# Performance work log

Hardware: AMD Instinct MI355X
Metric: run time of the kernel (lower is better)

Reference implementation:

```python
import jax, jax.numpy as jnp
import numpy as np

N_EXPERTS = 8
TOP_K = 2
AUX_COEF = 0.01
Z_COEF = 0.001


def setup_inputs() -> dict:
    key = jax.random.key(0)
    ks = jax.random.split(key, 5)
    B, S, D, F, E = 2, 2048, 768, 2048, N_EXPERTS
    std = 0.02
    std_out = std / np.sqrt(2 * 12)  # scale_init_by_depth, n_layers=12
    return {
        "x": jax.random.normal(ks[0], (B, S, D), jnp.float32),
        "router_w": jax.random.normal(ks[1], (D, E), jnp.float32) * std,
        "w1": jax.random.normal(ks[2], (E, D, F), jnp.float32) * std,
        "w2": jax.random.normal(ks[3], (E, F, D), jnp.float32) * std_out,
        "w3": jax.random.normal(ks[4], (E, D, F), jnp.float32) * std,
    }


def reference(x, router_w, w1, w2, w3):
    B, S, D = x.shape
    E = w1.shape[0]
    x_flat = x.reshape(-1, D)                      # [N, D]
    n_tokens = x_flat.shape[0]

    router_logits = x_flat @ router_w               # [N, E]
    probs = jax.nn.softmax(router_logits.astype(jnp.float32), axis=-1)
    topk_w, topk_i = jax.lax.top_k(probs, TOP_K)    # [N, K]
    topk_w = topk_w / jnp.sum(topk_w, axis=-1, keepdims=True)

    # Combine: equivalent to sort/group dispatch + per-expert GEMM + index_add,
    # expressed as a masked per-expert (fixed, small E) dense pass.
    out = jnp.zeros((n_tokens, D), dtype=x.dtype)
    for e in range(E):
        gate = jnp.sum(jnp.where(topk_i == e, topk_w, 0.0), axis=-1)  # [N] f32
        h = jax.nn.silu(x_flat @ w1[e]) * (x_flat @ w3[e])            # [N, F]
        out = out + gate[:, None].astype(x.dtype) * (h @ w2[e])

    # Switch-style load-balancing aux loss + z-loss
    importance = probs.mean(axis=0)                 # [E]
    top1 = topk_i[:, 0]
    load = jnp.zeros((E,), jnp.float32).at[top1].add(1.0) / n_tokens
    aux_loss = E * jnp.sum(importance * load) * AUX_COEF
    z_loss = jnp.mean(router_logits.astype(jnp.float32) ** 2) * Z_COEF

    return out.reshape(B, S, D), aux_loss, z_loss
```

## Files before the change

### kernel.cpp

```cpp
#include <hip/hip_runtime.h>
#include <hip/hip_bf16.h>

constexpr int NT = 4096;
constexpr int DD = 768;
constexpr int FF = 2048;
constexpr int NE = 8;
constexpr int MAXROWS = 9216;
constexpr int MAXMT128 = 72;

constexpr int IDX_CNTA   = 0;
constexpr int IDX_CNTT1  = 8;
constexpr int IDX_CUR    = 16;
constexpr int IDX_IMP    = 24;
constexpr int IDX_ZSUM   = 32;
constexpr int IDX_NTILES = 33;
constexpr int IDX_OFF    = 34;
constexpr int IDX_EXPT   = 48;

constexpr size_t OFF_META   = 0;
constexpr size_t OFF_TKE    = 1024;
constexpr size_t OFF_GATE   = OFF_TKE    + (size_t)NT*2*4;
constexpr size_t OFF_ROWOF  = OFF_GATE   + (size_t)NT*2*4;
constexpr size_t OFF_TOKROW = OFF_ROWOF  + (size_t)NT*2*4;
constexpr size_t OFF_XG     = 136192;
constexpr size_t OFF_W1T    = OFF_XG  + (size_t)MAXROWS*DD*2;
constexpr size_t OFF_W3T    = OFF_W1T + (size_t)NE*FF*DD*2;
constexpr size_t OFF_W2T    = OFF_W3T + (size_t)NE*FF*DD*2;
constexpr size_t OFF_H      = OFF_W2T + (size_t)NE*FF*DD*2;
constexpr size_t OFF_OP     = OFF_H   + (size_t)MAXROWS*FF*2;

typedef float f32x4 __attribute__((ext_vector_type(4)));
typedef __bf16 bf16x8v __attribute__((ext_vector_type(8)));
typedef unsigned short u16x8 __attribute__((ext_vector_type(8)));

__device__ inline unsigned short f2bf_bits(float f) {
  __bf16 h = (__bf16)f;
  return *(unsigned short*)&h;
}
__device__ inline float bf2f(unsigned short u) {
  unsigned v = (unsigned)u << 16;
  return *(float*)&v;
}

__device__ __forceinline__ void glds16(const void* g, void* l) {
  __builtin_amdgcn_global_load_lds(
      (const __attribute__((address_space(1))) unsigned int*)g,
      (__attribute__((address_space(3))) unsigned int*)l, 16, 0, 0);
}

constexpr int RB = 128;
__global__ __launch_bounds__(256) void router_kernel(const float* __restrict__ x,
    const float* __restrict__ rw, int* __restrict__ meta,
    int* __restrict__ tke, float* __restrict__ gateArr,
    int* __restrict__ tokrow) {
  const int gtid = blockIdx.x * 256 + threadIdx.x;
  if (gtid < MAXROWS) tokrow[gtid] = -1;

  __shared__ float s_imp[NE];
  __shared__ float s_z;
  __shared__ int s_cnt1[NE], s_cnta[NE];
  if (threadIdx.x < NE) { s_imp[threadIdx.x] = 0.f; s_cnt1[threadIdx.x] = 0; s_cnta[threadIdx.x] = 0; }
  if (threadIdx.x == 0) s_z = 0.f;
  __syncthreads();

  const int wave = threadIdx.x >> 6, lane = threadIdx.x & 63;
  float impacc[NE];
  #pragma unroll
  for (int e = 0; e < NE; ++e) impacc[e] = 0.f;
  float zacc = 0.f;

  for (int t = blockIdx.x * 4 + wave; t < NT; t += RB * 4) {
    float acc[NE];
    #pragma unroll
    for (int e = 0; e < NE; ++e) acc[e] = 0.f;
    const float* xr = x + (size_t)t * DD;
    for (int i = lane; i < DD / 4; i += 64) {
      float4 xv = ((const float4*)xr)[i];
      const float* r = rw + i * 4 * NE;
      #pragma unroll
      for (int e = 0; e < NE; ++e) acc[e] += xv.x * r[e];
      #pragma unroll
      for (int e = 0; e < NE; ++e) acc[e] += xv.y * r[NE + e];
      #pragma unroll
      for (int e = 0; e < NE; ++e) acc[e] += xv.z * r[2*NE + e];
      #pragma unroll
      for (int e = 0; e < NE; ++e) acc[e] += xv.w * r[3*NE + e];
    }
    #pragma unroll
    for (int off = 32; off > 0; off >>= 1) {
      #pragma unroll
      for (int e = 0; e < NE; ++e) acc[e] += __shfl_xor(acc[e], off);
    }
    float mx = acc[0];
    #pragma unroll
    for (int e = 1; e < NE; ++e) mx = fmaxf(mx, acc[e]);
    float p[NE]; float s = 0.f;
    #pragma unroll
    for (int e = 0; e < NE; ++e) { p[e] = __expf(acc[e] - mx); s += p[e]; }
    float inv = 1.f / s;
    #pragma unroll
    for (int e = 0; e < NE; ++e) p[e] *= inv;
    int e0 = 0; float p0 = p[0];
    #pragma unroll
    for (int e = 1; e < NE; ++e) if (p[e] > p0) { p0 = p[e]; e0 = e; }
    int e1 = -1; float p1 = -1.f;
    #pragma unroll
    for (int e = 0; e < NE; ++e) if (e != e0 && p[e] > p1) { p1 = p[e]; e1 = e; }
    if (lane == 0) {
      #pragma unroll
      for (int e = 0; e < NE; ++e) { impacc[e] += p[e]; zacc += acc[e] * acc[e]; }
      atomicAdd(&s_cnt1[e0], 1);
      atomicAdd(&s_cnta[e0], 1);
      atomicAdd(&s_cnta[e1], 1);
      float gs = 1.f / (p0 + p1);
      tke[t*2]   = e0; tke[t*2+1] = e1;
      gateArr[t*2] = p0 * gs; gateArr[t*2+1] = p1 * gs;
    }
  }
  if (lane == 0) {
    #pragma unroll
    for (int e = 0; e < NE; ++e) atomicAdd(&s_imp[e], impacc[e]);
    atomicAdd(&s_z, zacc);
  }
  __syncthreads();
  float* fmeta = (float*)meta;
  if (threadIdx.x < NE) {
    atomicAdd(&fmeta[IDX_IMP + threadIdx.x], s_imp[threadIdx.x]);
    atomicAdd(&meta[IDX_CNTT1 + threadIdx.x], s_cnt1[threadIdx.x]);
    atomicAdd(&meta[IDX_CNTA + threadIdx.x], s_cnta[threadIdx.x]);
  }
  if (threadIdx.x == NE) atomicAdd(&fmeta[IDX_ZSUM], s_z);
}

__global__ __launch_bounds__(128) void scan_kernel(int* __restrict__ meta,
                                                   float* __restrict__ out_tail) {
  __shared__ int s_off[NE + 1];
  __shared__ int s_nt[NE];
  __shared__ float s_aux;
  const int t = threadIdx.x;
  if (t < NE) s_nt[t] = (meta[IDX_CNTA + t] + 127) >> 7;
  __syncthreads();
  if (t == 0) {
    int off = 0;
    for (int e = 0; e < NE; ++e) { s_off[e] = off; off += s_nt[e]; }
    s_off[NE] = off;
  }
  __syncthreads();
  const int ntiles = s_off[NE];
  if (t < NE) meta[IDX_OFF + t] = s_off[t] << 7;
  if (t == NE) { meta[IDX_OFF + NE] = ntiles << 7; meta[IDX_NTILES] = ntiles; }
  if (t < ntiles) {
    int e = 0;
    while (t >= s_off[e + 1]) e++;
    meta[IDX_EXPT + t] = e;
  }
  float* fmeta = (float*)meta;
  float pl = 0.f;
  if (t < NE)
    pl = (fmeta[IDX_IMP + t] / (float)NT) * ((float)meta[IDX_CNTT1 + t] / (float)NT);
  if (t < 64) {
    #pragma unroll
    for (int off = 4; off > 0; off >>= 1) pl += __shfl_xor(pl, off);
    if (t == 0) s_aux = pl;
  }
  __syncthreads();
  if (t == 0) {
    out_tail[0] = (float)NE * s_aux * 0.01f;
    out_tail[1] = fmeta[IDX_ZSUM] / (float)(NT * NE) * 0.001f;
  }
}

__global__ __launch_bounds__(256) void scatter_kernel(const int* __restrict__ tke,
    int* __restrict__ meta, int* __restrict__ rowof, int* __restrict__ tokrow) {
  __shared__ int s_cnt[NE], s_base[NE];
  const int t = blockIdx.x * 256 + threadIdx.x;
  if (threadIdx.x < NE) s_cnt[threadIdx.x] = 0;
  __syncthreads();
  const int e0 = tke[t*2], e1 = tke[t*2 + 1];
  const int l0 = atomicAdd(&s_cnt[e0], 1);
  const int l1 = atomicAdd(&s_cnt[e1], 1);
  __syncthreads();
  if (threadIdx.x < NE)
    s_base[threadIdx.x] = atomicAdd(&meta[IDX_CUR + threadIdx.x], s_cnt[threadIdx.x]);
  __syncthreads();
  const int r0 = meta[IDX_OFF + e0] + s_base[e0] + l0;
  const int r1 = meta[IDX_OFF + e1] + s_base[e1] + l1;
  rowof[t*2]     = r0;
  rowof[t*2 + 1] = r1;
  tokrow[r0] = t;
  tokrow[r1] = t;
}

__global__ __launch_bounds__(192) void gather_kernel(const float* __restrict__ x,
    const int* __restrict__ tokrow, const int* __restrict__ meta,
    __bf16* __restrict__ Xg) {
  const int row = blockIdx.x;
  if (row >= meta[IDX_OFF + NE]) return;
  const int tok = tokrow[row];
  ushort4* dst = (ushort4*)(Xg + (size_t)row * DD);
  const int i = threadIdx.x;
  ushort4 o;
  if (tok >= 0) {
    float4 v = ((const float4*)(x + (size_t)tok * DD))[i];
    o.x = f2bf_bits(v.x); o.y = f2bf_bits(v.y);
    o.z = f2bf_bits(v.z); o.w = f2bf_bits(v.w);
  } else {
    o.x = o.y = o.z = o.w = 0;
  }
  dst[i] = o;
}

constexpr int TS = 68;
__global__ __launch_bounds__(256) void transpose_cvt_all(
    const float* __restrict__ w1, const float* __restrict__ w3,
    const float* __restrict__ w2, __bf16* __restrict__ W1t,
    __bf16* __restrict__ W3t, __bf16* __restrict__ W2t,
    int* __restrict__ meta) {
  if (blockIdx.x == 0 && blockIdx.y == 0 && blockIdx.z == 0)
    meta[threadIdx.x] = 0;

  const int z = blockIdx.z, which = z >> 3, e = z & 7;
  const float* src; __bf16* dst; int R, C;
  int r0a, c0a, r0b, c0b;
  if (which == 0)      { src = w1; dst = W1t; R = DD; C = FF;
                         r0a = blockIdx.y * 64; c0a = blockIdx.x * 128;
                         r0b = r0a;             c0b = c0a + 64; }
  else if (which == 1) { src = w3; dst = W3t; R = DD; C = FF;
                         r0a = blockIdx.y * 64; c0a = blockIdx.x * 128;
                         r0b = r0a;             c0b = c0a + 64; }
  else                 { src = w2; dst = W2t; R = FF; C = DD;
                         r0a = blockIdx.x * 128; c0a = blockIdx.y * 64;
                         r0b = r0a + 64;         c0b = c0a; }
  src += (size_t)e * DD * FF; dst += (size_t)e * DD * FF;
  __shared__ __align__(16) __bf16 tile[64 * TS];
  const int t = threadIdx.x;
  const int rr = t >> 4, qq = t & 15;

  float4 va[4], vb[4];
  #pragma unroll
  for (int i = 0; i < 4; ++i)
    va[i] = *(const float4*)&src[(size_t)(r0a + rr + i * 16) * C + c0a + qq * 4];
  #pragma unroll
  for (int i = 0; i < 4; ++i)
    vb[i] = *(const float4*)&src[(size_t)(r0b + rr + i * 16) * C + c0b + qq * 4];

  #pragma unroll
  for (int i = 0; i < 4; ++i) {
    ushort4 o;
    o.x = f2bf_bits(va[i].x); o.y = f2bf_bits(va[i].y);
    o.z = f2bf_bits(va[i].z); o.w = f2bf_bits(va[i].w);
    *(ushort4*)&tile[(rr + i * 16) * TS + qq * 4] = o;
  }
  __syncthreads();
  #pragma unroll
  for (int i = 0; i < 2; ++i) {
    int idx = t + i * 256; int c = idx >> 3, seg = idx & 7;
    u16x8 o;
    #pragma unroll
    for (int k = 0; k < 8; ++k)
      o[k] = *(unsigned short*)&tile[(seg * 8 + k) * TS + c];
    *(u16x8*)&dst[(size_t)(c0a + c) * R + r0a + seg * 8] = o;
  }
  __syncthreads();

  #pragma unroll
  for (int i = 0; i < 4; ++i) {
    ushort4 o;
    o.x = f2bf_bits(vb[i].x); o.y = f2bf_bits(vb[i].y);
    o.z = f2bf_bits(vb[i].z); o.w = f2bf_bits(vb[i].w);
    *(ushort4*)&tile[(rr + i * 16) * TS + qq * 4] = o;
  }
  __syncthreads();
  #pragma unroll
  for (int i = 0; i < 2; ++i) {
    int idx = t + i * 256; int c = idx >> 3, seg = idx & 7;
    u16x8 o;
    #pragma unroll
    for (int k = 0; k < 8; ++k)
      o[k] = *(unsigned short*)&tile[(seg * 8 + k) * TS + c];
    *(u16x8*)&dst[(size_t)(c0b + c) * R + r0b + seg * 8] = o;
  }
}

__global__ __launch_bounds__(256) void gemm1_kernel(const __bf16* __restrict__ Xg,
    const __bf16* __restrict__ W1t, const __bf16* __restrict__ W3t,
    __bf16* __restrict__ Hb, const int* __restrict__ meta) {
  const int mt = blockIdx.y;
  if (mt >= meta[IDX_NTILES]) return;
  const int e = meta[IDX_EXPT + mt];
  const int n0 = blockIdx.x * 64;
  const int m0 = mt * 128;
  __shared__ __align__(16) __bf16 As[128*32], B1s[64*32], B3s[64*32];
  const int t = threadIdx.x, wave = t >> 6, lane = t & 63;
  const __bf16* w1e = W1t + (size_t)e * FF * DD;
  const __bf16* w3e = W3t + (size_t)e * FF * DD;
  const f32x4 zero = {0.f, 0.f, 0.f, 0.f};
  f32x4 acc1[2][4], acc3[2][4];
  #pragma unroll
  for (int i = 0; i < 2; ++i)
    #pragma unroll
    for (int j = 0; j < 4; ++j) { acc1[i][j] = zero; acc3[i][j] = zero; }

  const __bf16* gA  = Xg  + (size_t)(m0 + 32*wave + (lane >> 2)) * DD + (lane & 3) * 8;
  const __bf16* gB1 = w1e + (size_t)(n0 + 16*wave + (lane >> 2)) * DD + (lane & 3) * 8;
  const __bf16* gB3 = w3e + (size_t)(n0 + 16*wave + (lane >> 2)) * DD + (lane & 3) * 8;
  __bf16* lA0 = &As [(32*wave     ) * 32];
  __bf16* lA1 = &As [(32*wave + 16) * 32];
  __bf16* lB1 = &B1s[(16*wave     ) * 32];
  __bf16* lB3 = &B3s[(16*wave     ) * 32];

  for (int k0 = 0; k0 < DD; k0 += 32) {
    glds16(gA  + k0,           lA0);
    glds16(gA  + k0 + 16*DD,   lA1);
    glds16(gB1 + k0,           lB1);
    glds16(gB3 + k0,           lB3);
    __syncthreads();
    bf16x8v a[2], b1[4], b3[4];
    #pragma unroll
    for (int i = 0; i < 2; ++i)
      a[i] = *(const bf16x8v*)&As[(32*wave + 16*i + (lane & 15))*32 + (lane >> 4)*8];
    #pragma unroll
    for (int j = 0; j < 4; ++j) {
      b1[j] = *(const bf16x8v*)&B1s[(16*j + (lane & 15))*32 + (lane >> 4)*8];
      b3[j] = *(const bf16x8v*)&B3s[(16*j + (lane & 15))*32 + (lane >> 4)*8];
    }
    #pragma unroll
    for (int i = 0; i < 2; ++i)
      #pragma unroll
      for (int j = 0; j < 4; ++j) {
        acc1[i][j] = __builtin_amdgcn_mfma_f32_16x16x32_bf16(a[i], b1[j], acc1[i][j], 0, 0, 0);
        acc3[i][j] = __builtin_amdgcn_mfma_f32_16x16x32_bf16(a[i], b3[j], acc3[i][j], 0, 0, 0);
      }
    __syncthreads();
  }
  #pragma unroll
  for (int i = 0; i < 2; ++i) {
    const int rowb = m0 + 32*wave + 16*i + (lane >> 4)*4;
    #pragma unroll
    for (int j = 0; j < 4; ++j) {
      const int col = n0 + 16*j + (lane & 15);
      #pragma unroll
      for (int r = 0; r < 4; ++r) {
        float c1 = acc1[i][j][r], c3 = acc3[i][j][r];
        float h = c1 / (1.f + __expf(-c1)) * c3;
        Hb[(size_t)(rowb + r)*FF + col] = (__bf16)h;
      }
    }
  }
}

__global__ __launch_bounds__(256) void gemm2_kernel(const __bf16* __restrict__ Hb,
    const __bf16* __restrict__ W2t, __bf16* __restrict__ OP,
    const int* __restrict__ meta) {
  const int mt = blockIdx.y;
  if (mt >= meta[IDX_NTILES]) return;
  const int e = meta[IDX_EXPT + mt];
  const int n0 = blockIdx.x * 128;
  const int m0 = mt * 128;
  __shared__ __align__(16) __bf16 As[128*32], Bs[128*32];
  const int t = threadIdx.x, wave = t >> 6, lane = t & 63;
  const int wm = wave & 1, wn = wave >> 1;
  const __bf16* w2e = W2t + (size_t)e * DD * FF;
  const f32x4 zero = {0.f, 0.f, 0.f, 0.f};
  f32x4 acc[4][4];
  #pragma unroll
  for (int i = 0; i < 4; ++i)
    #pragma unroll
    for (int j = 0; j < 4; ++j) acc[i][j] = zero;

  const __bf16* gA = Hb  + (size_t)(m0 + 32*wave + (lane >> 2)) * FF + (lane & 3) * 8;
  const __bf16* gB = w2e + (size_t)(n0 + 32*wave + (lane >> 2)) * FF + (lane & 3) * 8;
  __bf16* lA0 = &As[(32*wave     ) * 32];
  __bf16* lA1 = &As[(32*wave + 16) * 32];
  __bf16* lB0 = &Bs[(32*wave     ) * 32];
  __bf16* lB1 = &Bs[(32*wave + 16) * 32];

  for (int k0 = 0; k0 < FF; k0 += 32) {
    glds16(gA + k0,          lA0);
    glds16(gA + k0 + 16*FF,  lA1);
    glds16(gB + k0,          lB0);
    glds16(gB + k0 + 16*FF,  lB1);
    __syncthreads();
    bf16x8v a[4], b[4];
    #pragma unroll
    for (int i = 0; i < 4; ++i) {
      a[i] = *(const bf16x8v*)&As[(64*wm + 16*i + (lane & 15))*32 + (lane >> 4)*8];
      b[i] = *(const bf16x8v*)&Bs[(64*wn + 16*i + (lane & 15))*32 + (lane >> 4)*8];
    }
    #pragma unroll
    for (int i = 0; i < 4; ++i)
      #pragma unroll
      for (int j = 0; j < 4; ++j)
        acc[i][j] = __builtin_amdgcn_mfma_f32_16x16x32_bf16(a[i], b[j], acc[i][j], 0, 0, 0);
    __syncthreads();
  }
  #pragma unroll
  for (int i = 0; i < 4; ++i) {
    const int rowb = m0 + 64*wm + 16*i + (lane >> 4)*4;
    #pragma unroll
    for (int j = 0; j < 4; ++j) {
      const int col = n0 + 64*wn + 16*j + (lane & 15);
      #pragma unroll
      for (int r = 0; r < 4; ++r)
        OP[(size_t)(rowb + r)*DD + col] = (__bf16)acc[i][j][r];
    }
  }
}

__global__ __launch_bounds__(192) void combine_kernel(const __bf16* __restrict__ OP,
    const int* __restrict__ rowof, const float* __restrict__ gateArr,
    float* __restrict__ out) {
  const int t = blockIdx.x;
  const int r0 = rowof[t*2], r1 = rowof[t*2 + 1];
  const float g0 = gateArr[t*2], g1 = gateArr[t*2 + 1];
  const ushort4* p0 = (const ushort4*)(OP + (size_t)r0 * DD);
  const ushort4* p1 = (const ushort4*)(OP + (size_t)r1 * DD);
  const int i = threadIdx.x;
  ushort4 a = p0[i], b = p1[i];
  float4 o;
  o.x = g0 * bf2f(a.x) + g1 * bf2f(b.x);
  o.y = g0 * bf2f(a.y) + g1 * bf2f(b.y);
  o.z = g0 * bf2f(a.z) + g1 * bf2f(b.z);
  o.w = g0 * bf2f(a.w) + g1 * bf2f(b.w);
  ((float4*)(out + (size_t)t * DD))[i] = o;
}

extern "C" void kernel_launch(void* const* d_in, const int* in_sizes, int n_in,
                              void* d_out, int out_size, void* d_ws, size_t ws_size,
                              hipStream_t stream) {
  const float* x  = (const float*)d_in[0];
  const float* rw = (const float*)d_in[1];
  const float* w1 = (const float*)d_in[2];
  const float* w2 = (const float*)d_in[3];
  const float* w3 = (const float*)d_in[4];
  float* out = (float*)d_out;

  char* ws = (char*)d_ws;
  int*    meta   = (int*)(ws + OFF_META);
  int*    tke    = (int*)(ws + OFF_TKE);
  float*  gateA  = (float*)(ws + OFF_GATE);
  int*    rowof  = (int*)(ws + OFF_ROWOF);
  int*    tokrow = (int*)(ws + OFF_TOKROW);
  __bf16* Xg     = (__bf16*)(ws + OFF_XG);
  __bf16* W1t    = (__bf16*)(ws + OFF_W1T);
  __bf16* W3t    = (__bf16*)(ws + OFF_W3T);
  __bf16* W2t    = (__bf16*)(ws + OFF_W2T);
  __bf16* Hb     = (__bf16*)(ws + OFF_H);
  __bf16* OP     = (__bf16*)(ws + OFF_OP);

  transpose_cvt_all<<<dim3(16, 12, 24), 256, 0, stream>>>(w1, w3, w2,
                                                          W1t, W3t, W2t, meta);
  router_kernel<<<RB, 256, 0, stream>>>(x, rw, meta, tke, gateA, tokrow);
  scan_kernel<<<1, 128, 0, stream>>>(meta, out + (size_t)NT * DD);
  scatter_kernel<<<NT/256, 256, 0, stream>>>(tke, meta, rowof, tokrow);
  gather_kernel<<<MAXROWS, 192, 0, stream>>>(x, tokrow, meta, Xg);

  gemm1_kernel<<<dim3(FF/64, MAXMT128), 256, 0, stream>>>(Xg, W1t, W3t, Hb, meta);
  gemm2_kernel<<<dim3(DD/128, MAXMT128), 256, 0, stream>>>(Hb, W2t, OP, meta);
  combine_kernel<<<NT, 192, 0, stream>>>(OP, rowof, gateA, out);
}
```

Measured before the change: 352.9 us.

## Rewrite gemm2 with 256x128 tiles, double-buffered LDS and swizzled layout

The down-projection GEMM now uses 512-thread blocks computing 256x128 tiles with BK=64. The scan kernel builds a per-expert 256-row tile table, and a row limit masks stores that would spill into the next expert. Global-to-LDS loads are double-buffered with explicit vmcnt waits, LDS is XOR-swizzled to avoid bank conflicts, and s_setprio is raised around the MFMA bursts. The goal is more reuse of each W2 load, fewer barriers per FLOP and overlap of loads with compute, at the cost of more padded work in partially filled tiles and higher register and LDS use.

```diff
diff --git a/kernel.cpp b/kernel.cpp
--- a/kernel.cpp
+++ b/kernel.cpp
@@ -7,6 +7,8 @@
 constexpr int NE = 8;
 constexpr int MAXROWS = 9216;
 constexpr int MAXMT128 = 72;
+constexpr int MAXMT256 = 40;
+constexpr int NKT2 = FF / 64;
 
 constexpr int IDX_CNTA   = 0;
 constexpr int IDX_CNTT1  = 8;
@@ -16,6 +18,10 @@
 constexpr int IDX_NTILES = 33;
 constexpr int IDX_OFF    = 34;
 constexpr int IDX_EXPT   = 48;
+constexpr int IDX_N256   = 120;
+constexpr int IDX_E256   = 128;
+constexpr int IDX_B256   = 168;
+constexpr int IDX_L256   = 208;
 
 constexpr size_t OFF_META   = 0;
 constexpr size_t OFF_TKE    = 1024;
@@ -153,6 +159,21 @@
     int e = 0;
     while (t >= s_off[e + 1]) e++;
     meta[IDX_EXPT + t] = e;
+  }
+  if (t == 0) {
+    int n2t = 0;
+    for (int e = 0; e < NE; ++e) {
+      const int base = s_off[e] << 7;
+      const int lim  = base + (s_nt[e] << 7);
+      const int n2 = (s_nt[e] + 1) >> 1;
+      for (int i = 0; i < n2; ++i) {
+        meta[IDX_E256 + n2t] = e;
+        meta[IDX_B256 + n2t] = base + (i << 8);
+        meta[IDX_L256 + n2t] = lim;
+        ++n2t;
+      }
+    }
+    meta[IDX_N256] = n2t;
   }
   float* fmeta = (float*)meta;
   float pl = 0.f;
@@ -349,60 +370,136 @@
   }
 }
 
-__global__ __launch_bounds__(256) void gemm2_kernel(const __bf16* __restrict__ Hb,
-    const __bf16* __restrict__ W2t, __bf16* __restrict__ OP,
-    const int* __restrict__ meta) {
+__global__ __launch_bounds__(512, 2) void gemm2_kernel(
+    const __bf16* __restrict__ Hb, const __bf16* __restrict__ W2t,
+    __bf16* __restrict__ OP, const int* __restrict__ meta) {
   const int mt = blockIdx.y;
-  if (mt >= meta[IDX_NTILES]) return;
-  const int e = meta[IDX_EXPT + mt];
+  if (mt >= meta[IDX_N256]) return;
+  const int e      = meta[IDX_E256 + mt];
+  const int m0     = meta[IDX_B256 + mt];
+  const int rowlim = meta[IDX_L256 + mt];
   const int n0 = blockIdx.x * 128;
-  const int m0 = mt * 128;
-  __shared__ __align__(16) __bf16 As[128*32], Bs[128*32];
-  const int t = threadIdx.x, wave = t >> 6, lane = t & 63;
-  const int wm = wave & 1, wn = wave >> 1;
-  const __bf16* w2e = W2t + (size_t)e * DD * FF;
+
+  __shared__ __align__(16) __bf16 As[2][256 * 64];
+  __shared__ __align__(16) __bf16 Bs[2][128 * 64];
+
+  const int t = threadIdx.x, lane = t & 63, wid = t >> 6;
+  const int wm = wid >> 2, wn = wid & 3;
+  const int lane15 = lane & 15, g = lane >> 4;
+
+  const __bf16* __restrict__ W2e = W2t + (size_t)e * DD * FF;
+
+  const int aBase = (wm * 128 + lane15) * 64;
+  const int bBase = (wn * 32 + lane15) * 64;
+  const int c0 = ((g    ) ^ (lane & 7)) * 8;
+  const int c1 = ((4 + g) ^ (lane & 7)) * 8;
+
+  const int o0v = t, o1v = 512 + t;
+  const int r0v = o0v >> 3, r1v = o1v >> 3;
+  const int cl0 = (o0v & 7) ^ (r0v & 7), cl1 = (o1v & 7) ^ (r1v & 7);
+  const int L00 = (       wid * 64) * 8;
+  const int L01 = ( 512 + wid * 64) * 8;
+  const int L10 = (1024 + wid * 64) * 8;
+  const int L11 = (1536 + wid * 64) * 8;
+
+  int gA00 = m0 + r0v;        if (gA00 >= MAXROWS) gA00 = 0;
+  int gA01 = m0 + r1v;        if (gA01 >= MAXROWS) gA01 = 0;
+  int gA10 = m0 + 128 + r0v;  if (gA10 >= MAXROWS) gA10 = 0;
+  int gA11 = m0 + 128 + r1v;  if (gA11 >= MAXROWS) gA11 = 0;
+  const __bf16* aS00 = Hb + (size_t)gA00 * FF + cl0 * 8;
+  const __bf16* aS01 = Hb + (size_t)gA01 * FF + cl1 * 8;
+  const __bf16* aS10 = Hb + (size_t)gA10 * FF + cl0 * 8;
+  const __bf16* aS11 = Hb + (size_t)gA11 * FF + cl1 * 8;
+  const __bf16* bS0  = W2e + (size_t)(n0 + r0v) * FF + cl0 * 8;
+  const __bf16* bS1  = W2e + (size_t)(n0 + r1v) * FF + cl1 * 8;
+
+  auto stA = [&](__bf16* d, int kt) {
+    glds16(aS00 + (size_t)kt * 64, d + L00);
+    glds16(aS01 + (size_t)kt * 64, d + L01);
+    glds16(aS10 + (size_t)kt * 64, d + L10);
+    glds16(aS11 + (size_t)kt * 64, d + L11);
+  };
+  auto stB = [&](__bf16* d, int kt) {
+    glds16(bS0 + (size_t)kt * 64, d + L00);
+    glds16(bS1 + (size_t)kt * 64, d + L01);
+  };
+
   const f32x4 zero = {0.f, 0.f, 0.f, 0.f};
-  f32x4 acc[4][4];
-  #pragma unroll
-  for (int i = 0; i < 4; ++i)
-    #pragma unroll
-    for (int j = 0; j < 4; ++j) acc[i][j] = zero;
-
-  const __bf16* gA = Hb  + (size_t)(m0 + 32*wave + (lane >> 2)) * FF + (lane & 3) * 8;
-  const __bf16* gB = w2e + (size_t)(n0 + 32*wave + (lane >> 2)) * FF + (lane & 3) * 8;
-  __bf16* lA0 = &As[(32*wave     ) * 32];
-  __bf16* lA1 = &As[(32*wave + 16) * 32];
-  __bf16* lB0 = &Bs[(32*wave     ) * 32];
-  __bf16* lB1 = &Bs[(32*wave + 16) * 32];
-
-  for (int k0 = 0; k0 < FF; k0 += 32) {
-    glds16(gA + k0,          lA0);
-    glds16(gA + k0 + 16*FF,  lA1);
-    glds16(gB + k0,          lB0);
-    glds16(gB + k0 + 16*FF,  lB1);
-    __syncthreads();
-    bf16x8v a[4], b[4];
+  f32x4 acc[8][2];
+  #pragma unroll
+  for (int i = 0; i < 8; ++i)
+    #pragma unroll
+    for (int j = 0; j < 2; ++j) acc[i][j] = zero;
+
+  __bf16 *Ac = &As[0][0], *An = &As[1][0];
+  __bf16 *Bc = &Bs[0][0], *Bn = &Bs[1][0];
+
+  stA(Ac, 0); stB(Bc, 0);
+  stA(An, 1); stB(Bn, 1);
+  asm volatile("s_waitcnt vmcnt(6)" ::: "memory");
+  __builtin_amdgcn_s_barrier();
+
+  bf16x8v af[8], ag[8], bfr[4];
+
+  for (int k = 0; k < NKT2; ++k) {
+    const bool k2ok = (k < NKT2 - 2);
     #pragma unroll
     for (int i = 0; i < 4; ++i) {
-      a[i] = *(const bf16x8v*)&As[(64*wm + 16*i + (lane & 15))*32 + (lane >> 4)*8];
-      b[i] = *(const bf16x8v*)&Bs[(64*wn + 16*i + (lane & 15))*32 + (lane >> 4)*8];
-    }
+      af[i*2+0] = *(const bf16x8v*)&Ac[aBase + i*1024 + c0];
+      af[i*2+1] = *(const bf16x8v*)&Ac[aBase + i*1024 + c1];
+    }
+    #pragma unroll
+    for (int i = 0; i < 4; ++i) {
+      ag[i*2+0] = *(const bf16x8v*)&Ac[aBase + (4+i)*1024 + c0];
+      ag[i*2+1] = *(const bf16x8v*)&Ac[aBase + (4+i)*1024 + c1];
+    }
+    #pragma unroll
+    for (int j = 0; j < 2; ++j) {
+      bfr[j*2+0] = *(const bf16x8v*)&Bc[bBase + j*1024 + c0];
+      bfr[j*2+1] = *(const bf16x8v*)&Bc[bBase + j*1024 + c1];
+    }
+    __builtin_amdgcn_s_barrier();
+    asm volatile("s_waitcnt lgkmcnt(0)" ::: "memory");
+    __builtin_amdgcn_s_setprio(1);
     #pragma unroll
     for (int i = 0; i < 4; ++i)
       #pragma unroll
-      for (int j = 0; j < 4; ++j)
-        acc[i][j] = __builtin_amdgcn_mfma_f32_16x16x32_bf16(a[i], b[j], acc[i][j], 0, 0, 0);
-    __syncthreads();
-  }
-  #pragma unroll
-  for (int i = 0; i < 4; ++i) {
-    const int rowb = m0 + 64*wm + 16*i + (lane >> 4)*4;
-    #pragma unroll
-    for (int j = 0; j < 4; ++j) {
-      const int col = n0 + 64*wn + 16*j + (lane & 15);
+      for (int j = 0; j < 2; ++j) {
+        acc[i][j] = __builtin_amdgcn_mfma_f32_16x16x32_bf16(af[i*2+0], bfr[j*2+0], acc[i][j], 0, 0, 0);
+        acc[i][j] = __builtin_amdgcn_mfma_f32_16x16x32_bf16(af[i*2+1], bfr[j*2+1], acc[i][j], 0, 0, 0);
+      }
+    __builtin_amdgcn_s_setprio(0);
+    __builtin_amdgcn_s_barrier();
+
+    if (k2ok) { stA(Ac, k + 2); stB(Bc, k + 2); }
+    __builtin_amdgcn_s_setprio(1);
+    #pragma unroll
+    for (int i = 0; i < 4; ++i)
+      #pragma unroll
+      for (int j = 0; j < 2; ++j) {
+        acc[4+i][j] = __builtin_amdgcn_mfma_f32_16x16x32_bf16(ag[i*2+0], bfr[j*2+0], acc[4+i][j], 0, 0, 0);
+        acc[4+i][j] = __builtin_amdgcn_mfma_f32_16x16x32_bf16(ag[i*2+1], bfr[j*2+1], acc[4+i][j], 0, 0, 0);
+      }
+    __builtin_amdgcn_s_setprio(0);
+    if (k2ok)               { asm volatile("s_waitcnt vmcnt(6)" ::: "memory"); }
+    else if (k == NKT2 - 2) { asm volatile("s_waitcnt vmcnt(0)" ::: "memory"); }
+    __builtin_amdgcn_s_barrier();
+
+    __bf16* tp;
+    tp = Ac; Ac = An; An = tp;
+    tp = Bc; Bc = Bn; Bn = tp;
+  }
+
+  #pragma unroll
+  for (int i = 0; i < 8; ++i) {
+    const int rowb = m0 + wm * 128 + i * 16 + (lane >> 4) * 4;
+    #pragma unroll
+    for (int jj = 0; jj < 2; ++jj) {
+      const int col = n0 + wn * 32 + jj * 16 + lane15;
       #pragma unroll
       for (int r = 0; r < 4; ++r)
-        OP[(size_t)(rowb + r)*DD + col] = (__bf16)acc[i][j][r];
+        if (rowb + r < rowlim)
+          OP[(size_t)(rowb + r) * DD + col] = (__bf16)acc[i][jj][r];
     }
   }
 }
@@ -456,6 +553,6 @@
   gather_kernel<<<MAXROWS, 192, 0, stream>>>(x, tokrow, meta, Xg);
 
   gemm1_kernel<<<dim3(FF/64, MAXMT128), 256, 0, stream>>>(Xg, W1t, W3t, Hb, meta);
-  gemm2_kernel<<<dim3(DD/128, MAXMT128), 256, 0, stream>>>(Hb, W2t, OP, meta);
+  gemm2_kernel<<<dim3(DD/128, MAXMT256), 512, 0, stream>>>(Hb, W2t, OP, meta);
   combine_kernel<<<NT, 192, 0, stream>>>(OP, rowof, gateA, out);
 }
```

Result: no change. 355.2 us (+0.6%).
